# Kernel optimization log

Hardware: AMD Instinct MI355X
Metric: run time of the kernel (lower is better)

Reference implementation:

```python
import jax, jax.numpy as jnp
import numpy as np

NUM_HEADS = 16


def setup_inputs() -> dict:
    key = jax.random.key(0)
    ks = jax.random.split(key, 7)
    B, N, D = 16, 512, 1024
    return {
        "x": jax.random.normal(ks[0], (B, N, D), dtype=jnp.float32),
        "spatial_encoding": jax.random.normal(ks[1], (B, N, N), dtype=jnp.float32),
        "edge_encoding": jax.random.normal(ks[2], (B, N, N), dtype=jnp.float32),
        "Wq": jax.random.normal(ks[3], (D, D), dtype=jnp.float32) * (D ** -0.5),
        "Wk": jax.random.normal(ks[4], (D, D), dtype=jnp.float32) * (D ** -0.5),
        "Wv": jax.random.normal(ks[5], (D, D), dtype=jnp.float32) * (D ** -0.5),
        "Wo": jax.random.normal(ks[6], (D, D), dtype=jnp.float32) * (D ** -0.5),
    }


def reference(x, spatial_encoding, edge_encoding, Wq, Wk, Wv, Wo):
    B, N, D = x.shape
    H = NUM_HEADS
    hd = D // H
    scale = D ** -0.5  # NOTE: source scales by hidden_dim**-0.5, not head_size**-0.5

    def split_heads(t):  # (B,N,D) -> (B,H,N,hd)
        return t.reshape(B, N, H, hd).transpose(0, 2, 1, 3)

    q = split_heads(x @ Wq.T)
    k = split_heads(x @ Wk.T)
    v = split_heads(x @ Wv.T)

    bias = (spatial_encoding + edge_encoding)[:, None]  # (B,1,N,N)
    a = jnp.einsum("bhnd,bhmd->bhnm", q, k) * scale + bias  # (B,H,N,N)

    # rows that are entirely zero (padded) are masked to -inf
    row_nonzero = jnp.any(a != 0, axis=-1, keepdims=True)  # (B,H,N,1)
    a = jnp.where(row_nonzero, a, -jnp.inf)
    p = jax.nn.softmax(a, axis=-1)
    p = jnp.where(jnp.isnan(p), 0.0, p)  # nan_to_num after softmax of all -inf rows

    o = jnp.einsum("bhnm,bhmd->bhnd", p, v)  # (B,H,N,hd)
    o = o.transpose(0, 2, 1, 3).reshape(B, N, D)
    return o @ Wo.T
```

## Files before the change

kernel.cpp:

```cpp
#include <hip/hip_runtime.h>
#include <cstdint>


typedef unsigned short u16;
typedef unsigned int   u32;
typedef __attribute__((ext_vector_type(8))) short bf8;
typedef __attribute__((ext_vector_type(4))) float f4;

__device__ __forceinline__ u16 f2bf(float x) {
  u32 u = __float_as_uint(x);
  u += 0x7FFF + ((u >> 16) & 1);
  return (u16)(u >> 16);
}

__device__ __forceinline__ float bf2f(u16 x) {
  return __uint_as_float(((u32)x) << 16);
}

__device__ __forceinline__ void gl2lds16(const void* g, void* l) {
  __builtin_amdgcn_global_load_lds(
      (const __attribute__((address_space(1))) u32*)g,
      (__attribute__((address_space(3))) u32*)l, 16, 0, 0);
}


__global__ __launch_bounds__(256) void cast_bf16(const float* __restrict__ src,
                                                 uint4* __restrict__ dst, int n8) {
  const int i = blockIdx.x * 256 + threadIdx.x;
  if (i >= n8) return;
  const float4* s = (const float4*)src;
  const float4 a = s[2 * i], c = s[2 * i + 1];
  uint4 o;
  o.x = (u32)f2bf(a.x) | ((u32)f2bf(a.y) << 16);
  o.y = (u32)f2bf(a.z) | ((u32)f2bf(a.w) << 16);
  o.z = (u32)f2bf(c.x) | ((u32)f2bf(c.y) << 16);
  o.w = (u32)f2bf(c.z) | ((u32)f2bf(c.w) << 16);
  dst[i] = o;
}

__global__ __launch_bounds__(256) void cast4_bf16(
    const float* __restrict__ s0, const float* __restrict__ s1,
    const float* __restrict__ s2, const float* __restrict__ s3,
    uint4* __restrict__ d0, uint4* __restrict__ d1,
    uint4* __restrict__ d2, uint4* __restrict__ d3) {
  const int i = blockIdx.x * 256 + threadIdx.x;
  const int w = i >> 17, j = i & 131071;
  const float* src = (w == 0) ? s0 : (w == 1) ? s1 : (w == 2) ? s2 : s3;
  uint4* dst = (w == 0) ? d0 : (w == 1) ? d1 : (w == 2) ? d2 : d3;
  const float4* s = (const float4*)src;
  const float4 a = s[2 * j], c = s[2 * j + 1];
  uint4 o;
  o.x = (u32)f2bf(a.x) | ((u32)f2bf(a.y) << 16);
  o.y = (u32)f2bf(a.z) | ((u32)f2bf(a.w) << 16);
  o.z = (u32)f2bf(c.x) | ((u32)f2bf(c.y) << 16);
  o.w = (u32)f2bf(c.z) | ((u32)f2bf(c.w) << 16);
  dst[j] = o;
}

__global__ __launch_bounds__(256) void bias_perm(const float* __restrict__ sp,
                                                 const float* __restrict__ ed,
                                                 u16* __restrict__ Bp) {
  const int jt = blockIdx.x, qt = blockIdx.y, b = blockIdx.z;
  const int tid = threadIdx.x;
  const int wave = tid >> 6, quad = (tid >> 4) & 3, l16 = tid & 15;
  const int qrl = (wave << 4) + (quad << 2);
  union { u16 a[16]; uint4 v[2]; } tmp;
#pragma unroll
  for (int nb = 0; nb < 4; nb++) {
    const int col = (jt << 6) + (nb << 4) + l16;
#pragma unroll
    for (int r = 0; r < 4; r++) {
      const int row = (qt << 6) + qrl + r;
      const size_t idx = ((size_t)b << 18) + (size_t)row * 512 + col;
      tmp.a[nb * 4 + r] = f2bf(sp[idx] + ed[idx]);
    }
  }
  uint4* out = (uint4*)Bp + ((((size_t)b * 8 + qt) * 8 + jt) * 256 + tid) * 2;
  out[0] = tmp.v[0];
  out[1] = tmp.v[1];
}


__device__ __forceinline__ void gemm_core(const u16* __restrict__ A,
                                          const u16* __restrict__ Bt,
                                          int m0, int n0,
                                          u16* lA, u16* lB, f4 acc[4][4]) {
  const int tid  = threadIdx.x;
  const int wave = tid >> 6;
  const int lane = tid & 63;
  const int quad = lane >> 4;
  const int l16  = lane & 15;
  const int wm   = (wave >> 1) << 6;
  const int wn   = (wave & 1) << 6;
  const int srow = tid >> 3;
  const int scol = ((tid & 7) ^ (srow & 7)) << 3;
  const int c0   = (quad ^ (l16 & 7)) << 3;

  f4 zero = {0.f, 0.f, 0.f, 0.f};
#pragma unroll
  for (int mi = 0; mi < 4; mi++)
#pragma unroll
    for (int ni = 0; ni < 4; ni++) acc[mi][ni] = zero;

  const u16* Ab = A  + (size_t)(m0 + srow) * 1024 + scol;
  const u16* Bb = Bt + (size_t)(n0 + srow) * 1024 + scol;

  for (int k0 = 0; k0 < 1024; k0 += 64) {
    __syncthreads();
#pragma unroll
    for (int i = 0; i < 4; i++) {
      gl2lds16(Ab + (size_t)(i << 5) * 1024 + k0,
               (char*)lA + (((i << 8) + (wave << 6)) << 4));
      gl2lds16(Bb + (size_t)(i << 5) * 1024 + k0,
               (char*)lB + (((i << 8) + (wave << 6)) << 4));
    }
    __syncthreads();
#pragma unroll
    for (int kk = 0; kk < 64; kk += 32) {
      const int o = c0 ^ kk;
      bf8 af[4], bfr[4];
#pragma unroll
      for (int mi = 0; mi < 4; mi++)
        af[mi] = *(const bf8*)(lA + (wm + (mi << 4) + l16) * 64 + o);
#pragma unroll
      for (int ni = 0; ni < 4; ni++)
        bfr[ni] = *(const bf8*)(lB + (wn + (ni << 4) + l16) * 64 + o);
#pragma unroll
      for (int mi = 0; mi < 4; mi++)
#pragma unroll
        for (int ni = 0; ni < 4; ni++)
          acc[mi][ni] = __builtin_amdgcn_mfma_f32_16x16x32_bf16(
              af[mi], bfr[ni], acc[mi][ni], 0, 0, 0);
    }
  }
}


__global__ __launch_bounds__(256) void qkv_kernel(
    const u16* __restrict__ xb, const u16* __restrict__ wq,
    const u16* __restrict__ wk, const u16* __restrict__ wv,
    u16* __restrict__ Qh, u16* __restrict__ Kh, u16* __restrict__ Vt) {
  __shared__ __align__(16) u16 lA[128 * 64];
  __shared__ __align__(16) u16 lB[128 * 64];
  const int flat = blockIdx.x + (blockIdx.y << 3) + (blockIdx.z << 9);
  const int m_tile = (flat & 7) | (((flat >> 6) & 7) << 3);
  const int n_tile = (flat >> 3) & 7;
  const int proj = flat >> 9;
  const int m0 = m_tile << 7, n0 = n_tile << 7;
  const u16* W = (proj == 0) ? wq : (proj == 1) ? wk : wv;
  f4 acc[4][4];
  gemm_core(xb, W, m0, n0, lA, lB, acc);

  const int tid = threadIdx.x, wave = tid >> 6, lane = tid & 63;
  const int quad = lane >> 4, l16 = lane & 15;
  const int wm = (wave >> 1) << 6, wn = (wave & 1) << 6;

  if (proj == 2) {
#pragma unroll
    for (int mi = 0; mi < 4; mi++) {
      const int gmb = m0 + wm + (mi << 4) + (quad << 2);
      const int b = gmb >> 9, nb = gmb & 511;
#pragma unroll
      for (int ni = 0; ni < 4; ni++) {
        const int gn = n0 + wn + (ni << 4) + l16;
        const int h = gn >> 6, hdi = gn & 63;
        ushort4 pk;
        pk.x = f2bf(acc[mi][ni][0]);
        pk.y = f2bf(acc[mi][ni][1]);
        pk.z = f2bf(acc[mi][ni][2]);
        pk.w = f2bf(acc[mi][ni][3]);
        *(ushort4*)(Vt + ((size_t)((b << 4) + h) * 64 + hdi) * 512 + nb) = pk;
      }
    }
  } else {
    u16* dst = (proj == 0) ? Qh : Kh;
#pragma unroll
    for (int mi = 0; mi < 4; mi++) {
#pragma unroll
      for (int r = 0; r < 4; r++) {
        const int gm = m0 + wm + (mi << 4) + (quad << 2) + r;
        const int b = gm >> 9, n = gm & 511;
#pragma unroll
        for (int ni = 0; ni < 4; ni++) {
          const int gn = n0 + wn + (ni << 4) + l16;
          const int h = gn >> 6, hdi = gn & 63;
          dst[((size_t)((b << 4) + h) * 512 + n) * 64 + hdi] = f2bf(acc[mi][ni][r]);
        }
      }
    }
  }
}


__global__ __launch_bounds__(256) void oproj_kernel(const u16* __restrict__ Ob,
                                                    const u16* __restrict__ wo,
                                                    float* __restrict__ out) {
  __shared__ __align__(16) u16 lA[128 * 64];
  __shared__ __align__(16) u16 lB[128 * 64];
  const int flat = blockIdx.x + (blockIdx.y << 3);
  const int m0 = ((flat & 7) | (((flat >> 6) & 7) << 3)) << 7;
  const int n0 = ((flat >> 3) & 7) << 7;
  f4 acc[4][4];
  gemm_core(Ob, wo, m0, n0, lA, lB, acc);

  const int tid = threadIdx.x, wave = tid >> 6, lane = tid & 63;
  const int quad = lane >> 4, l16 = lane & 15;
  const int wm = (wave >> 1) << 6, wn = (wave & 1) << 6;
#pragma unroll
  for (int mi = 0; mi < 4; mi++)
#pragma unroll
    for (int r = 0; r < 4; r++) {
      const int gm = m0 + wm + (mi << 4) + (quad << 2) + r;
#pragma unroll
      for (int ni = 0; ni < 4; ni++) {
        const int gn = n0 + wn + (ni << 4) + l16;
        out[(size_t)gm * 1024 + gn] = acc[mi][ni][r];
      }
    }
}


__global__ __launch_bounds__(256) void attn_kernel(
    const u16* __restrict__ Qh, const u16* __restrict__ Kh,
    const u16* __restrict__ Vt, const u16* __restrict__ Bp,
    u16* __restrict__ Ob) {
  __shared__ __align__(16) u16 sQ[64 * 64];
  __shared__ __align__(16) u16 sK[64 * 64];
  __shared__ __align__(16) u16 sV[64 * 64];
  __shared__ __align__(16) u16 sP[4 * 16 * 72];
  const int flat = blockIdx.x + (blockIdx.y << 3) + (blockIdx.z << 7);
  const int qt = (flat >> 3) & 7;
  const int h  = (flat >> 6) & 15;
  const int b  = (flat & 7) | (((flat >> 10) & 1) << 3);
  const int q0 = qt << 6;
  const int tid = threadIdx.x, wave = tid >> 6, lane = tid & 63;
  const int quad = lane >> 4, l16 = lane & 15;
  const int c0  = (quad ^ (l16 & 7)) << 3;
  const int swb = (((tid & 7) ^ ((tid >> 3) & 7)) << 4);

  const u16* Qg = Qh + ((size_t)((b << 4) + h) * 512 + q0) * 64;
  const u16* Kg = Kh + (size_t)((b << 4) + h) * 512 * 64;
  const u16* Vg = Vt + (size_t)((b << 4) + h) * 64 * 512;
  const uint4* Bpg = (const uint4*)Bp + (((size_t)b * 8 + qt) * 8 * 256 + tid) * 2;

#pragma unroll
  for (int i = 0; i < 2; i++) {
    const int e = (i << 8) + tid;
    gl2lds16((const char*)Qg + (e >> 3) * 128 + swb,
             (char*)sQ + (((i << 8) + (wave << 6)) << 4));
  }

  f4 o[4];
  f4 zero = {0.f, 0.f, 0.f, 0.f};
#pragma unroll
  for (int i = 0; i < 4; i++) o[i] = zero;
  float lsum[4] = {0.f, 0.f, 0.f, 0.f};
  const int qrl = (wave << 4) + (quad << 2);

  for (int j0 = 0; j0 < 512; j0 += 64) {
    const uint4 bc0 = Bpg[(j0 >> 6) * 512];
    const uint4 bc1 = Bpg[(j0 >> 6) * 512 + 1];
    const u32 bw[8] = {bc0.x, bc0.y, bc0.z, bc0.w, bc1.x, bc1.y, bc1.z, bc1.w};

    __syncthreads();
#pragma unroll
    for (int i = 0; i < 2; i++) {
      const int e = (i << 8) + tid;
      gl2lds16((const char*)Kg + (size_t)j0 * 128 + (e >> 3) * 128 + swb,
               (char*)sK + (((i << 8) + (wave << 6)) << 4));
      gl2lds16((const char*)Vg + (size_t)(e >> 3) * 1024 + j0 * 2 + swb,
               (char*)sV + (((i << 8) + (wave << 6)) << 4));
    }
    __syncthreads();

    bf8 aq0 = *(const bf8*)(sQ + ((wave << 4) + l16) * 64 + c0);
    bf8 aq1 = *(const bf8*)(sQ + ((wave << 4) + l16) * 64 + (c0 ^ 32));
    u16* pw = sP + wave * (16 * 72);
#pragma unroll
    for (int nb = 0; nb < 4; nb++) {
      bf8 b0 = *(const bf8*)(sK + ((nb << 4) + l16) * 64 + c0);
      bf8 b1 = *(const bf8*)(sK + ((nb << 4) + l16) * 64 + (c0 ^ 32));
      f4 s = zero;
      s = __builtin_amdgcn_mfma_f32_16x16x32_bf16(aq0, b0, s, 0, 0, 0);
      s = __builtin_amdgcn_mfma_f32_16x16x32_bf16(aq1, b1, s, 0, 0, 0);
#pragma unroll
      for (int r = 0; r < 4; r++) {
        const u32 w = bw[nb * 2 + (r >> 1)];
        const float bias = bf2f((r & 1) ? (u16)(w >> 16) : (u16)(w & 0xFFFF));
        const float ev = __expf(s[r] * 0.03125f + bias);
        lsum[r] += ev;
        pw[((quad << 2) + r) * 72 + (nb << 4) + l16] = f2bf(ev);
      }
    }

    bf8 ap0 = *(const bf8*)(pw + l16 * 72 + (quad << 3));
    bf8 ap1 = *(const bf8*)(pw + l16 * 72 + 32 + (quad << 3));
#pragma unroll
    for (int db = 0; db < 4; db++) {
      bf8 v0 = *(const bf8*)(sV + ((db << 4) + l16) * 64 + c0);
      bf8 v1 = *(const bf8*)(sV + ((db << 4) + l16) * 64 + (c0 ^ 32));
      o[db] = __builtin_amdgcn_mfma_f32_16x16x32_bf16(ap0, v0, o[db], 0, 0, 0);
      o[db] = __builtin_amdgcn_mfma_f32_16x16x32_bf16(ap1, v1, o[db], 0, 0, 0);
    }
  }

#pragma unroll
  for (int r = 0; r < 4; r++) {
    float s = lsum[r];
    s += __shfl_xor(s, 1);
    s += __shfl_xor(s, 2);
    s += __shfl_xor(s, 4);
    s += __shfl_xor(s, 8);
    const float inv = 1.f / s;
    const int gr = q0 + qrl + r;
#pragma unroll
    for (int db = 0; db < 4; db++)
      Ob[(size_t)((b << 9) + gr) * 1024 + (h << 6) + (db << 4) + l16] =
          f2bf(o[db][r] * inv);
  }
}


extern "C" void kernel_launch(void* const* d_in, const int* in_sizes, int n_in,
                              void* d_out, int out_size, void* d_ws, size_t ws_size,
                              hipStream_t stream) {
  const float* x  = (const float*)d_in[0];
  const float* sp = (const float*)d_in[1];
  const float* ed = (const float*)d_in[2];
  const float* Wq = (const float*)d_in[3];
  const float* Wk = (const float*)d_in[4];
  const float* Wv = (const float*)d_in[5];
  const float* Wo = (const float*)d_in[6];
  float* out = (float*)d_out;

  char* w = (char*)d_ws;
  u16* xb  = (u16*)(w);
  u16* wqb = (u16*)(w + 16777216);
  u16* wkb = (u16*)(w + 18874368);
  u16* wvb = (u16*)(w + 20971520);
  u16* wob = (u16*)(w + 23068672);
  u16* Qh  = (u16*)(w + 25165824);
  u16* Kh  = (u16*)(w + 41943040);
  u16* Vt  = (u16*)(w + 58720256);
  u16* Ob  = (u16*)(w + 75497472);
  u16* Bp  = (u16*)(w + 92274688);

  cast_bf16<<<4096, 256, 0, stream>>>(x, (uint4*)xb, 1048576);
  cast4_bf16<<<2048, 256, 0, stream>>>(Wq, Wk, Wv, Wo,
                                       (uint4*)wqb, (uint4*)wkb,
                                       (uint4*)wvb, (uint4*)wob);
  bias_perm<<<dim3(8, 8, 16), 256, 0, stream>>>(sp, ed, Bp);

  qkv_kernel<<<dim3(8, 64, 3), 256, 0, stream>>>(xb, wqb, wkb, wvb, Qh, Kh, Vt);
  attn_kernel<<<dim3(8, 16, 16), 256, 0, stream>>>(Qh, Kh, Vt, Bp, Ob);
  oproj_kernel<<<dim3(8, 64, 1), 256, 0, stream>>>(Ob, wob, out);
}
```

Measured before the change: 251.5 us.

## Double-buffer K/V loads in attention and vectorize GEMM epilogue stores

```diff
diff --git a/kernel.cpp b/kernel.cpp
--- a/kernel.cpp
+++ b/kernel.cpp
@@ -21,6 +21,12 @@
   __builtin_amdgcn_global_load_lds(
       (const __attribute__((address_space(1))) u32*)g,
       (__attribute__((address_space(3))) u32*)l, 16, 0, 0);
+}
+
+__device__ __forceinline__ void barrier_raw() {
+  asm volatile("" ::: "memory");
+  __builtin_amdgcn_s_barrier();
+  asm volatile("" ::: "memory");
 }
 
 
@@ -81,6 +87,7 @@
 }
 
 
+template <bool SWAP>
 __device__ __forceinline__ void gemm_core(const u16* __restrict__ A,
                                           const u16* __restrict__ Bt,
                                           int m0, int n0,
@@ -128,9 +135,14 @@
 #pragma unroll
       for (int mi = 0; mi < 4; mi++)
 #pragma unroll
-        for (int ni = 0; ni < 4; ni++)
-          acc[mi][ni] = __builtin_amdgcn_mfma_f32_16x16x32_bf16(
-              af[mi], bfr[ni], acc[mi][ni], 0, 0, 0);
+        for (int ni = 0; ni < 4; ni++) {
+          if (SWAP)
+            acc[mi][ni] = __builtin_amdgcn_mfma_f32_16x16x32_bf16(
+                bfr[ni], af[mi], acc[mi][ni], 0, 0, 0);
+          else
+            acc[mi][ni] = __builtin_amdgcn_mfma_f32_16x16x32_bf16(
+                af[mi], bfr[ni], acc[mi][ni], 0, 0, 0);
+        }
     }
   }
 }
@@ -148,14 +160,14 @@
   const int proj = flat >> 9;
   const int m0 = m_tile << 7, n0 = n_tile << 7;
   const u16* W = (proj == 0) ? wq : (proj == 1) ? wk : wv;
-  f4 acc[4][4];
-  gemm_core(xb, W, m0, n0, lA, lB, acc);
 
   const int tid = threadIdx.x, wave = tid >> 6, lane = tid & 63;
   const int quad = lane >> 4, l16 = lane & 15;
   const int wm = (wave >> 1) << 6, wn = (wave & 1) << 6;
+  f4 acc[4][4];
 
   if (proj == 2) {
+    gemm_core<false>(xb, W, m0, n0, lA, lB, acc);
 #pragma unroll
     for (int mi = 0; mi < 4; mi++) {
       const int gmb = m0 + wm + (mi << 4) + (quad << 2);
@@ -173,19 +185,22 @@
       }
     }
   } else {
+    gemm_core<true>(xb, W, m0, n0, lA, lB, acc);
     u16* dst = (proj == 0) ? Qh : Kh;
 #pragma unroll
     for (int mi = 0; mi < 4; mi++) {
-#pragma unroll
-      for (int r = 0; r < 4; r++) {
-        const int gm = m0 + wm + (mi << 4) + (quad << 2) + r;
-        const int b = gm >> 9, n = gm & 511;
-#pragma unroll
-        for (int ni = 0; ni < 4; ni++) {
-          const int gn = n0 + wn + (ni << 4) + l16;
-          const int h = gn >> 6, hdi = gn & 63;
-          dst[((size_t)((b << 4) + h) * 512 + n) * 64 + hdi] = f2bf(acc[mi][ni][r]);
-        }
+      const int gm = m0 + wm + (mi << 4) + l16;
+      const int b = gm >> 9, n = gm & 511;
+#pragma unroll
+      for (int ni = 0; ni < 4; ni++) {
+        const int gn = n0 + wn + (ni << 4) + (quad << 2);
+        const int h = gn >> 6, hdi = gn & 63;
+        ushort4 pk;
+        pk.x = f2bf(acc[mi][ni][0]);
+        pk.y = f2bf(acc[mi][ni][1]);
+        pk.z = f2bf(acc[mi][ni][2]);
+        pk.w = f2bf(acc[mi][ni][3]);
+        *(ushort4*)(dst + ((size_t)((b << 4) + h) * 512 + n) * 64 + hdi) = pk;
       }
     }
   }
@@ -201,22 +216,25 @@
   const int m0 = ((flat & 7) | (((flat >> 6) & 7) << 3)) << 7;
   const int n0 = ((flat >> 3) & 7) << 7;
   f4 acc[4][4];
-  gemm_core(Ob, wo, m0, n0, lA, lB, acc);
+  gemm_core<true>(Ob, wo, m0, n0, lA, lB, acc);
 
   const int tid = threadIdx.x, wave = tid >> 6, lane = tid & 63;
   const int quad = lane >> 4, l16 = lane & 15;
   const int wm = (wave >> 1) << 6, wn = (wave & 1) << 6;
 #pragma unroll
-  for (int mi = 0; mi < 4; mi++)
-#pragma unroll
-    for (int r = 0; r < 4; r++) {
-      const int gm = m0 + wm + (mi << 4) + (quad << 2) + r;
-#pragma unroll
-      for (int ni = 0; ni < 4; ni++) {
-        const int gn = n0 + wn + (ni << 4) + l16;
-        out[(size_t)gm * 1024 + gn] = acc[mi][ni][r];
-      }
-    }
+  for (int mi = 0; mi < 4; mi++) {
+    const int gm = m0 + wm + (mi << 4) + l16;
+#pragma unroll
+    for (int ni = 0; ni < 4; ni++) {
+      const int gn = n0 + wn + (ni << 4) + (quad << 2);
+      float4 f;
+      f.x = acc[mi][ni][0];
+      f.y = acc[mi][ni][1];
+      f.z = acc[mi][ni][2];
+      f.w = acc[mi][ni][3];
+      *(float4*)(out + (size_t)gm * 1024 + gn) = f;
+    }
+  }
 }
 
 
@@ -225,8 +243,8 @@
     const u16* __restrict__ Vt, const u16* __restrict__ Bp,
     u16* __restrict__ Ob) {
   __shared__ __align__(16) u16 sQ[64 * 64];
-  __shared__ __align__(16) u16 sK[64 * 64];
-  __shared__ __align__(16) u16 sV[64 * 64];
+  __shared__ __align__(16) u16 sK[2][64 * 64];
+  __shared__ __align__(16) u16 sV[2][64 * 64];
   __shared__ __align__(16) u16 sP[4 * 16 * 72];
   const int flat = blockIdx.x + (blockIdx.y << 3) + (blockIdx.z << 7);
   const int qt = (flat >> 3) & 7;
@@ -249,6 +267,19 @@
     gl2lds16((const char*)Qg + (e >> 3) * 128 + swb,
              (char*)sQ + (((i << 8) + (wave << 6)) << 4));
   }
+#pragma unroll
+  for (int i = 0; i < 2; i++) {
+    const int e = (i << 8) + tid;
+    gl2lds16((const char*)Kg + (e >> 3) * 128 + swb,
+             (char*)sK[0] + (((i << 8) + (wave << 6)) << 4));
+    gl2lds16((const char*)Vg + (size_t)(e >> 3) * 1024 + swb,
+             (char*)sV[0] + (((i << 8) + (wave << 6)) << 4));
+  }
+  asm volatile("s_waitcnt vmcnt(4)" ::: "memory");
+  barrier_raw();
+
+  const bf8 aq0 = *(const bf8*)(sQ + ((wave << 4) + l16) * 64 + c0);
+  const bf8 aq1 = *(const bf8*)(sQ + ((wave << 4) + l16) * 64 + (c0 ^ 32));
 
   f4 o[4];
   f4 zero = {0.f, 0.f, 0.f, 0.f};
@@ -257,29 +288,37 @@
   float lsum[4] = {0.f, 0.f, 0.f, 0.f};
   const int qrl = (wave << 4) + (quad << 2);
 
-  for (int j0 = 0; j0 < 512; j0 += 64) {
-    const uint4 bc0 = Bpg[(j0 >> 6) * 512];
-    const uint4 bc1 = Bpg[(j0 >> 6) * 512 + 1];
+  int cur = 0;
+  for (int jt = 0; jt < 8; jt++) {
+    const uint4 bc0 = Bpg[jt * 512];
+    const uint4 bc1 = Bpg[jt * 512 + 1];
     const u32 bw[8] = {bc0.x, bc0.y, bc0.z, bc0.w, bc1.x, bc1.y, bc1.z, bc1.w};
 
-    __syncthreads();
-#pragma unroll
-    for (int i = 0; i < 2; i++) {
-      const int e = (i << 8) + tid;
-      gl2lds16((const char*)Kg + (size_t)j0 * 128 + (e >> 3) * 128 + swb,
-               (char*)sK + (((i << 8) + (wave << 6)) << 4));
-      gl2lds16((const char*)Vg + (size_t)(e >> 3) * 1024 + j0 * 2 + swb,
-               (char*)sV + (((i << 8) + (wave << 6)) << 4));
-    }
-    __syncthreads();
-
-    bf8 aq0 = *(const bf8*)(sQ + ((wave << 4) + l16) * 64 + c0);
-    bf8 aq1 = *(const bf8*)(sQ + ((wave << 4) + l16) * 64 + (c0 ^ 32));
+    if (jt < 7) {
+      const int j1 = (jt + 1) << 6;
+#pragma unroll
+      for (int i = 0; i < 2; i++) {
+        const int e = (i << 8) + tid;
+        gl2lds16((const char*)Kg + (size_t)j1 * 128 + (e >> 3) * 128 + swb,
+                 (char*)sK[cur ^ 1] + (((i << 8) + (wave << 6)) << 4));
+        gl2lds16((const char*)Vg + (size_t)(e >> 3) * 1024 + j1 * 2 + swb,
+                 (char*)sV[cur ^ 1] + (((i << 8) + (wave << 6)) << 4));
+      }
+      asm volatile("s_waitcnt vmcnt(4)" ::: "memory");
+    } else {
+      asm volatile("s_waitcnt vmcnt(0)" ::: "memory");
+    }
+    barrier_raw();
+
+    const u16* kbuf = sK[cur];
+    const u16* vbuf = sV[cur];
     u16* pw = sP + wave * (16 * 72);
+
+    __builtin_amdgcn_s_setprio(1);
 #pragma unroll
     for (int nb = 0; nb < 4; nb++) {
-      bf8 b0 = *(const bf8*)(sK + ((nb << 4) + l16) * 64 + c0);
-      bf8 b1 = *(const bf8*)(sK + ((nb << 4) + l16) * 64 + (c0 ^ 32));
+      bf8 b0 = *(const bf8*)(kbuf + ((nb << 4) + l16) * 64 + c0);
+      bf8 b1 = *(const bf8*)(kbuf + ((nb << 4) + l16) * 64 + (c0 ^ 32));
       f4 s = zero;
       s = __builtin_amdgcn_mfma_f32_16x16x32_bf16(aq0, b0, s, 0, 0, 0);
       s = __builtin_amdgcn_mfma_f32_16x16x32_bf16(aq1, b1, s, 0, 0, 0);
@@ -292,16 +331,22 @@
         pw[((quad << 2) + r) * 72 + (nb << 4) + l16] = f2bf(ev);
       }
     }
+    __builtin_amdgcn_s_setprio(0);
 
     bf8 ap0 = *(const bf8*)(pw + l16 * 72 + (quad << 3));
     bf8 ap1 = *(const bf8*)(pw + l16 * 72 + 32 + (quad << 3));
+    __builtin_amdgcn_s_setprio(1);
 #pragma unroll
     for (int db = 0; db < 4; db++) {
-      bf8 v0 = *(const bf8*)(sV + ((db << 4) + l16) * 64 + c0);
-      bf8 v1 = *(const bf8*)(sV + ((db << 4) + l16) * 64 + (c0 ^ 32));
+      bf8 v0 = *(const bf8*)(vbuf + ((db << 4) + l16) * 64 + c0);
+      bf8 v1 = *(const bf8*)(vbuf + ((db << 4) + l16) * 64 + (c0 ^ 32));
       o[db] = __builtin_amdgcn_mfma_f32_16x16x32_bf16(ap0, v0, o[db], 0, 0, 0);
       o[db] = __builtin_amdgcn_mfma_f32_16x16x32_bf16(ap1, v1, o[db], 0, 0, 0);
     }
+    __builtin_amdgcn_s_setprio(0);
+
+    barrier_raw();
+    cur ^= 1;
   }
 
 #pragma unroll
```

Result: slower. 264.3 us (+5.1%).

## Swap MFMA operands for vectorized Q/K and output stores; keep Q in registers

Applied to the files above, without the earlier changes.

```diff
diff --git a/kernel.cpp b/kernel.cpp
--- a/kernel.cpp
+++ b/kernel.cpp
@@ -81,6 +81,7 @@
 }
 
 
+template <bool SWAP>
 __device__ __forceinline__ void gemm_core(const u16* __restrict__ A,
                                           const u16* __restrict__ Bt,
                                           int m0, int n0,
@@ -128,9 +129,14 @@
 #pragma unroll
       for (int mi = 0; mi < 4; mi++)
 #pragma unroll
-        for (int ni = 0; ni < 4; ni++)
-          acc[mi][ni] = __builtin_amdgcn_mfma_f32_16x16x32_bf16(
-              af[mi], bfr[ni], acc[mi][ni], 0, 0, 0);
+        for (int ni = 0; ni < 4; ni++) {
+          if (SWAP)
+            acc[mi][ni] = __builtin_amdgcn_mfma_f32_16x16x32_bf16(
+                bfr[ni], af[mi], acc[mi][ni], 0, 0, 0);
+          else
+            acc[mi][ni] = __builtin_amdgcn_mfma_f32_16x16x32_bf16(
+                af[mi], bfr[ni], acc[mi][ni], 0, 0, 0);
+        }
     }
   }
 }
@@ -148,14 +154,14 @@
   const int proj = flat >> 9;
   const int m0 = m_tile << 7, n0 = n_tile << 7;
   const u16* W = (proj == 0) ? wq : (proj == 1) ? wk : wv;
-  f4 acc[4][4];
-  gemm_core(xb, W, m0, n0, lA, lB, acc);
 
   const int tid = threadIdx.x, wave = tid >> 6, lane = tid & 63;
   const int quad = lane >> 4, l16 = lane & 15;
   const int wm = (wave >> 1) << 6, wn = (wave & 1) << 6;
+  f4 acc[4][4];
 
   if (proj == 2) {
+    gemm_core<false>(xb, W, m0, n0, lA, lB, acc);
 #pragma unroll
     for (int mi = 0; mi < 4; mi++) {
       const int gmb = m0 + wm + (mi << 4) + (quad << 2);
@@ -173,19 +179,22 @@
       }
     }
   } else {
+    gemm_core<true>(xb, W, m0, n0, lA, lB, acc);
     u16* dst = (proj == 0) ? Qh : Kh;
 #pragma unroll
     for (int mi = 0; mi < 4; mi++) {
-#pragma unroll
-      for (int r = 0; r < 4; r++) {
-        const int gm = m0 + wm + (mi << 4) + (quad << 2) + r;
-        const int b = gm >> 9, n = gm & 511;
-#pragma unroll
-        for (int ni = 0; ni < 4; ni++) {
-          const int gn = n0 + wn + (ni << 4) + l16;
-          const int h = gn >> 6, hdi = gn & 63;
-          dst[((size_t)((b << 4) + h) * 512 + n) * 64 + hdi] = f2bf(acc[mi][ni][r]);
-        }
+      const int gm = m0 + wm + (mi << 4) + l16;
+      const int b = gm >> 9, n = gm & 511;
+#pragma unroll
+      for (int ni = 0; ni < 4; ni++) {
+        const int gn = n0 + wn + (ni << 4) + (quad << 2);
+        const int h = gn >> 6, hdi = gn & 63;
+        ushort4 pk;
+        pk.x = f2bf(acc[mi][ni][0]);
+        pk.y = f2bf(acc[mi][ni][1]);
+        pk.z = f2bf(acc[mi][ni][2]);
+        pk.w = f2bf(acc[mi][ni][3]);
+        *(ushort4*)(dst + ((size_t)((b << 4) + h) * 512 + n) * 64 + hdi) = pk;
       }
     }
   }
@@ -201,30 +210,32 @@
   const int m0 = ((flat & 7) | (((flat >> 6) & 7) << 3)) << 7;
   const int n0 = ((flat >> 3) & 7) << 7;
   f4 acc[4][4];
-  gemm_core(Ob, wo, m0, n0, lA, lB, acc);
+  gemm_core<true>(Ob, wo, m0, n0, lA, lB, acc);
 
   const int tid = threadIdx.x, wave = tid >> 6, lane = tid & 63;
   const int quad = lane >> 4, l16 = lane & 15;
   const int wm = (wave >> 1) << 6, wn = (wave & 1) << 6;
 #pragma unroll
-  for (int mi = 0; mi < 4; mi++)
-#pragma unroll
-    for (int r = 0; r < 4; r++) {
-      const int gm = m0 + wm + (mi << 4) + (quad << 2) + r;
-#pragma unroll
-      for (int ni = 0; ni < 4; ni++) {
-        const int gn = n0 + wn + (ni << 4) + l16;
-        out[(size_t)gm * 1024 + gn] = acc[mi][ni][r];
-      }
-    }
-}
-
-
-__global__ __launch_bounds__(256) void attn_kernel(
+  for (int mi = 0; mi < 4; mi++) {
+    const int gm = m0 + wm + (mi << 4) + l16;
+#pragma unroll
+    for (int ni = 0; ni < 4; ni++) {
+      const int gn = n0 + wn + (ni << 4) + (quad << 2);
+      float4 f;
+      f.x = acc[mi][ni][0];
+      f.y = acc[mi][ni][1];
+      f.z = acc[mi][ni][2];
+      f.w = acc[mi][ni][3];
+      *(float4*)(out + (size_t)gm * 1024 + gn) = f;
+    }
+  }
+}
+
+
+__global__ __launch_bounds__(256, 5) void attn_kernel(
     const u16* __restrict__ Qh, const u16* __restrict__ Kh,
     const u16* __restrict__ Vt, const u16* __restrict__ Bp,
     u16* __restrict__ Ob) {
-  __shared__ __align__(16) u16 sQ[64 * 64];
   __shared__ __align__(16) u16 sK[64 * 64];
   __shared__ __align__(16) u16 sV[64 * 64];
   __shared__ __align__(16) u16 sP[4 * 16 * 72];
@@ -243,12 +254,8 @@
   const u16* Vg = Vt + (size_t)((b << 4) + h) * 64 * 512;
   const uint4* Bpg = (const uint4*)Bp + (((size_t)b * 8 + qt) * 8 * 256 + tid) * 2;
 
-#pragma unroll
-  for (int i = 0; i < 2; i++) {
-    const int e = (i << 8) + tid;
-    gl2lds16((const char*)Qg + (e >> 3) * 128 + swb,
-             (char*)sQ + (((i << 8) + (wave << 6)) << 4));
-  }
+  const bf8 aq0 = *(const bf8*)(Qg + ((wave << 4) + l16) * 64 + (quad << 3));
+  const bf8 aq1 = *(const bf8*)(Qg + ((wave << 4) + l16) * 64 + 32 + (quad << 3));
 
   f4 o[4];
   f4 zero = {0.f, 0.f, 0.f, 0.f};
@@ -273,8 +280,6 @@
     }
     __syncthreads();
 
-    bf8 aq0 = *(const bf8*)(sQ + ((wave << 4) + l16) * 64 + c0);
-    bf8 aq1 = *(const bf8*)(sQ + ((wave << 4) + l16) * 64 + (c0 ^ 32));
     u16* pw = sP + wave * (16 * 72);
 #pragma unroll
     for (int nb = 0; nb < 4; nb++) {
```

Measured after the change: 257.5 us. 2.4% more time.
